# Kernel optimization log

Hardware: AMD Instinct MI355X
Metric: run time of the kernel (lower is better)

The kernel has to match this reference:

```python
import jax, jax.numpy as jnp
import numpy as np

B, C, H, W = 16, 256, 32, 32
DIM = H * W  # LayerNorm/Linear dim == h*w per the rearrange in forward


def _conv1x1(x, w, b):
    # x: [b,c,h,w], w: [out,in] (1x1 kernel squeezed), b: [out]
    return jnp.einsum('bchw,oc->bohw', x, w) + b[None, :, None, None]


def _layernorm(x, g, b, eps=1e-5):
    mu = jnp.mean(x, axis=-1, keepdims=True)
    var = jnp.var(x, axis=-1, keepdims=True)
    return (x - mu) / jnp.sqrt(var + eps) * g + b


def setup_inputs() -> dict:
    key = jax.random.key(0)
    ks = jax.random.split(key, 12)
    n = jax.random.normal
    k_cdc = (2.0 / (2 * C)) ** 0.5   # kaiming_normal fan_in = 2C
    k_v = (2.0 / C) ** 0.5           # fan_in = C
    k_lin = (2.0 / DIM) ** 0.5       # fan_in = DIM
    return {
        'x_spa': n(ks[0], (B, C, H, W), jnp.float32),
        'x_freq': n(ks[1], (B, C, H, W), jnp.float32),
        'w_cdc': n(ks[2], (C, 2 * C), jnp.float32) * k_cdc,
        'b_cdc': jnp.zeros((C,), jnp.float32),
        'w_sv': n(ks[3], (C, C), jnp.float32) * k_v,
        'b_sv': jnp.zeros((C,), jnp.float32),
        'w_fv': n(ks[4], (C, C), jnp.float32) * k_v,
        'b_fv': jnp.zeros((C,), jnp.float32),
        'ln_w': jnp.ones((DIM,), jnp.float32),
        'ln_b': jnp.zeros((DIM,), jnp.float32),
        'w_qk': n(ks[5], (2 * DIM, DIM), jnp.float32) * k_lin,  # Linear(dim, 2*dim), no bias
        'w_spa': n(ks[6], (DIM, DIM), jnp.float32) * k_lin,
        'b_spa': jnp.zeros((DIM,), jnp.float32),
        'w_frq': n(ks[7], (DIM, DIM), jnp.float32) * k_lin,
        'b_frq': jnp.zeros((DIM,), jnp.float32),
    }


def reference(x_spa, x_freq, w_cdc, b_cdc, w_sv, b_sv, w_fv, b_fv,
              ln_w, ln_b, w_qk, w_spa, b_spa, w_frq, b_frq):
    b, c, h, w = x_spa.shape
    hw = h * w
    scale = hw ** (-0.5)
    v_spa = _conv1x1(x_spa, w_sv, b_sv).reshape(b, c, hw)
    v_freq = _conv1x1(x_freq, w_fv, b_fv).reshape(b, c, hw)
    x = _conv1x1(jnp.concatenate([x_spa, x_freq], axis=1), w_cdc, b_cdc).reshape(b, c, hw)
    x = _layernorm(x, ln_w, ln_b)
    qk = x @ w_qk.T                       # [b, c, 2*hw]
    q, k = jnp.split(qk, 2, axis=-1)      # each [b, c, hw]
    att = jnp.einsum('bcn,bcm->bnm', q, k) * scale   # q^T k over channels: [b, hw, hw]
    att_spa = jax.nn.softmax(att @ w_spa.T + b_spa, axis=-1)
    att_frq = jax.nn.softmax(att @ w_frq.T + b_frq, axis=-1)
    out_spa = x_spa + jnp.einsum('bcn,bnm->bcm', v_spa, att_spa).reshape(b, c, h, w)
    out_freq = x_freq + jnp.einsum('bcn,bnm->bcm', v_freq, att_frq).reshape(b, c, h, w)
    return out_spa, out_freq
```

## Files before the change

kernel.cpp:

```cpp
#include <hip/hip_runtime.h>
#include <hip/hip_bf16.h>

typedef __hip_bfloat16 bf16;
typedef __attribute__((ext_vector_type(8))) short bf16x8v;
typedef __attribute__((ext_vector_type(4))) float f32x4v;

__device__ __forceinline__ float bfbits2f(unsigned short h) {
    union { unsigned int u; float f; } v; v.u = ((unsigned int)h) << 16; return v.f;
}
__device__ __forceinline__ unsigned short f2bfbits(float f) {
    bf16 h = __float2bfloat16(f);
    unsigned short s;
    __builtin_memcpy(&s, &h, 2);
    return s;
}
__device__ __forceinline__ float load1_any(const void* p, long idx, bool f32) {
    if (f32) return ((const float*)p)[idx];
    return bfbits2f(((const unsigned short*)p)[idx]);
}
__device__ __forceinline__ float4 loadbf4(const bf16* p) {
    ushort4 u = *reinterpret_cast<const ushort4*>(p);
    return make_float4(bfbits2f(u.x), bfbits2f(u.y), bfbits2f(u.z), bfbits2f(u.w));
}
__device__ __forceinline__ void store_bf4(bf16* p, float a, float b, float c, float d) {
    ushort4 o;
    o.x = f2bfbits(a); o.y = f2bfbits(b); o.z = f2bfbits(c); o.w = f2bfbits(d);
    *reinterpret_cast<ushort4*>(p) = o;
}
__device__ __forceinline__ void gl16(const void* g, void* l) {
    __builtin_amdgcn_global_load_lds(
        (const __attribute__((address_space(1))) unsigned int*)g,
        (__attribute__((address_space(3))) unsigned int*)l, 16, 0, 0);
}
#define CMAX_INIT 0x00800000u

__global__ __launch_bounds__(1024)
void detect_kernel(const unsigned short* __restrict__ x, int* __restrict__ flag) {
    const int tid = threadIdx.x;
    int zc = 0, hc = 0;
    const uint4* xv = (const uint4*)x;
#pragma unroll
    for (int p = 0; p < 16; ++p) {
        uint4 v = xv[p * 1024 + tid];
        unsigned s0 = v.x & 0xFFFFu, s1 = v.y & 0xFFFFu;
        unsigned s2 = v.z & 0xFFFFu, s3 = v.w & 0xFFFFu;
        zc += (int)(s0 == 0) + (int)(s1 == 0) + (int)(s2 == 0) + (int)(s3 == 0);
        hc += (int)(((s0 >> 7) & 0xFFu) >= 0x90u) + (int)(((s1 >> 7) & 0xFFu) >= 0x90u)
            + (int)(((s2 >> 7) & 0xFFu) >= 0x90u) + (int)(((s3 >> 7) & 0xFFu) >= 0x90u);
    }
#pragma unroll
    for (int off = 32; off > 0; off >>= 1) {
        zc += __shfl_down(zc, off);
        hc += __shfl_down(hc, off);
    }
    __shared__ int rz[16], rh[16];
    if ((tid & 63) == 0) { rz[tid >> 6] = zc; rh[tid >> 6] = hc; }
    __syncthreads();
    if (tid == 0) {
        int Z = 0, H = 0;
#pragma unroll
        for (int i = 0; i < 16; ++i) { Z += rz[i]; H += rh[i]; }
        flag[0] = (Z > 60000 || H > 256) ? 1 : 0;
        flag[1] = 1;
    }
}

__global__ void diag_kernel(float* __restrict__ out, float val) {
    if (threadIdx.x == 0) out[0] = val;
}

__global__ __launch_bounds__(256)
void convert6_kernel(const void* __restrict__ s0, const void* __restrict__ s1,
                     const void* __restrict__ s2, const void* __restrict__ s3,
                     const void* __restrict__ s4, const void* __restrict__ s5,
                     const void* __restrict__ b0, const void* __restrict__ b1,
                     const void* __restrict__ b2,
                     bf16* __restrict__ dst, bf16* __restrict__ wl,
                     float* __restrict__ bc, const int* __restrict__ dflag) {
    const bool f32 = (*dflag != 0);
    for (long i = (long)blockIdx.x * 256 + threadIdx.x; i < 4850432;
         i += (long)gridDim.x * 256) {
        if (i < 4456448) {
            const void* s; long o;
            if (i < 131072)       { s = s0; o = i; }
            else if (i < 196608)  { s = s1; o = i - 131072; }
            else if (i < 262144)  { s = s2; o = i - 196608; }
            else if (i < 2359296) { s = s3; o = i - 262144; }
            else if (i < 3407872) { s = s4; o = i - 2359296; }
            else                  { s = s5; o = i - 3407872; }
            dst[i] = __float2bfloat16(load1_any(s, o, f32));
        } else if (i < 4849664) {
            long j = i - 4456448;
            int r = (int)(j >> 9), c = (int)(j & 511);
            float v = 0.f;
            if (r < 256) v = load1_any(s0, r * 512 + c, f32);
            else if (r < 512) { if (c < 256) v = load1_any(s1, (r - 256) * 256 + c, f32); }
            else              { if (c >= 256) v = load1_any(s2, (r - 512) * 256 + (c - 256), f32); }
            wl[j] = __float2bfloat16(v);
        } else {
            long j = i - 4849664;
            float v = (j < 256) ? load1_any(b0, j, f32)
                    : (j < 512) ? load1_any(b1, j - 256, f32)
                                : load1_any(b2, j - 512, f32);
            bc[j] = v;
        }
    }
}

__global__ __launch_bounds__(256)
void xpose_w_kernel(const bf16* __restrict__ src, bf16* __restrict__ dst) {
    __shared__ float t[64][65];
    const int c0 = blockIdx.x * 64, r0 = blockIdx.y * 64;
    const int tid = threadIdx.x;
#pragma unroll
    for (int p = 0; p < 16; ++p) {
        int e = tid + p * 256; int r = e >> 6, c = e & 63;
        t[r][c] = __bfloat162float(src[(long)(r0 + r) * 1024 + c0 + c]);
    }
    __syncthreads();
#pragma unroll
    for (int p = 0; p < 16; ++p) {
        int e = tid + p * 256; int r = e >> 6, c = e & 63;
        dst[(long)(c0 + r) * 1024 + r0 + c] = __float2bfloat16(t[c][r]);
    }
}

__global__ __launch_bounds__(256)
void xpose_conv_kernel(const void* __restrict__ x1, const void* __restrict__ x2,
                       bf16* __restrict__ dst, unsigned* __restrict__ colmax,
                       int bofs, int zsplit, const int* __restrict__ dflag) {
    const bool f32 = (*dflag != 0);
    __shared__ float t[64][65];
    const int ch0 = blockIdx.y * 64, n0 = blockIdx.x * 64, z = blockIdx.z;
    const bool hiz = (z >= zsplit);
    const int zl = hiz ? z - zsplit : z;
    const void* x = hiz ? x2 : x1;
    const long sb = (long)(zl + bofs) * 262144, db = (long)z * 262144;
    const int tid = threadIdx.x;
    if (blockIdx.x == 0 && blockIdx.y == 0) {
        uint4* ci = (uint4*)(colmax + (long)z * 1024) + tid;
        *ci = make_uint4(CMAX_INIT, CMAX_INIT, CMAX_INIT, CMAX_INIT);
    }
    if (f32) {
        const float* xf = (const float*)x;
#pragma unroll
        for (int p = 0; p < 4; ++p) {
            int e = tid + p * 256; int sch = e >> 4, sn = (e & 15) * 4;
            float4 v = *(const float4*)(xf + sb + (long)(ch0 + sch) * 1024 + n0 + sn);
            t[sch][sn] = v.x; t[sch][sn + 1] = v.y;
            t[sch][sn + 2] = v.z; t[sch][sn + 3] = v.w;
        }
    } else {
#pragma unroll
        for (int p = 0; p < 16; ++p) {
            int e = tid + p * 256; int sch = e >> 6, sn = e & 63;
            t[sch][sn] = bfbits2f(((const unsigned short*)x)[sb + (long)(ch0 + sch) * 1024 + n0 + sn]);
        }
    }
    __syncthreads();
#pragma unroll
    for (int p = 0; p < 16; ++p) {
        int e = tid + p * 256; int dn = e >> 6, dch = e & 63;
        dst[db + (long)(n0 + dn) * 256 + ch0 + dch] = __float2bfloat16(t[dch][dn]);
    }
}

__global__ __launch_bounds__(256)
void smnorm_kernel(bf16* __restrict__ X, bf16* __restrict__ vb,
                   const unsigned* __restrict__ colmax, int gN, int gq) {
    const int tid = threadIdx.x;
    const int cg = tid & 7;
    const int js = tid >> 3;
    const int n0 = blockIdx.x * 64;
    const long zb = (long)blockIdx.y * 1048576;
    unsigned short* Xp = (unsigned short*)X + zb + n0 + cg * 8;
    const unsigned* cm = colmax + (long)blockIdx.y * 1024 + n0 + cg * 8;

    float M8[8], s8[8];
#pragma unroll
    for (int q = 0; q < 8; ++q) {
        unsigned k = cm[q];
        unsigned b = (k & 0x80000000u) ? (k & 0x7fffffffu) : ~k;
        M8[q] = __uint_as_float(b);
        s8[q] = 0.f;
    }
#pragma unroll 4
    for (int r = 0; r < 32; ++r) {
        long off = (long)(js * 32 + r) * 1024;
        bf16x8v u = *(const bf16x8v*)(Xp + off);
        bf16x8v o;
#pragma unroll
        for (int q = 0; q < 8; ++q) {
            float e = __expf(bfbits2f((unsigned short)u[q]) - M8[q]);
            s8[q] += e;
            o[q] = (short)f2bfbits(e);
        }
        *(bf16x8v*)(Xp + off) = o;
    }
    __shared__ float sh[32][8][8];
    __shared__ float Sc[64];
#pragma unroll
    for (int q = 0; q < 8; ++q) sh[js][cg][q] = s8[q];
    __syncthreads();
    if (tid < 64) {
        float ss = 0.f;
#pragma unroll 8
        for (int s = 0; s < 32; ++s) ss += sh[s][tid >> 3][tid & 7];
        Sc[tid] = 1.0f / ss;
    }
    __syncthreads();
    const int side = (blockIdx.y >= (unsigned)gq) ? 1 : 0;
    const int zl = blockIdx.y - side * gq;
    bf16* vp = vb + (long)(side * 256) * gN + (long)zl * 1024 + n0 + cg * 8;
    float is8[8];
#pragma unroll
    for (int q = 0; q < 8; ++q) is8[q] = Sc[cg * 8 + q];
#pragma unroll
    for (int rr = 0; rr < 8; ++rr) {
        long off = (long)(rr * 32 + js) * gN;
        bf16x8v u = *(bf16x8v*)(vp + off);
        bf16x8v o;
#pragma unroll
        for (int q = 0; q < 8; ++q)
            o[q] = (short)f2bfbits(bfbits2f((unsigned short)u[q]) * is8[q]);
        *(bf16x8v*)(vp + off) = o;
    }
}

template <int MI, int EPI>
__global__ __launch_bounds__(256)
void mfma_nt(const bf16* __restrict__ A1, const bf16* __restrict__ A2,
             long aB1, long aB2, int ldA1, int ldA2,
             const bf16* __restrict__ B1, const bf16* __restrict__ B2,
             long bB1, long bB2, int ldB1, int ldB2,
             int ksplit, long kOff2,
             void* __restrict__ out1, void* __restrict__ out2,
             long oB1, long oB2, int ldO1, int ldO2,
             int K, float scale,
             const void* __restrict__ bias1, const void* __restrict__ bias2,
             const void* __restrict__ res1, const void* __restrict__ res2,
             long rBatch, int bofs, int zsplit,
             const int* __restrict__ dflag) {
    constexpr int BM = MI * 32;
    __shared__ short As[3][BM * 32];
    __shared__ short Bs[3][4096];
    const int tid  = threadIdx.x;
    const int lane = tid & 63, wave = tid >> 6;
    const int quad = lane >> 4, lrow = lane & 15;
    const int wm = (wave >> 1) * (MI * 16), wn = (wave & 1) * 64;

    int bx = blockIdx.x, by = blockIdx.y, bz = blockIdx.z;
    {
        const int gx = gridDim.x, gy = gridDim.y;
        const int gxy = gx * gy;
        const int ntot = gxy * gridDim.z;
        if ((ntot & 7) == 0) {
            int flat = bx + gx * (by + gy * bz);
            int w = (flat & 7) * (ntot >> 3) + (flat >> 3);
            bz = w / gxy;
            int rem = w - bz * gxy;
            by = rem / gx;
            bx = rem - by * gx;
        }
    }
    const int z  = bz;
    const bool hiz = (z >= zsplit);
    const int zl = hiz ? z - zsplit : z;
    const int n0 = bx * 128, m0 = by * BM;
    const int ldA = hiz ? ldA2 : ldA1, ldB = hiz ? ldB2 : ldB1;
    const int ldO = hiz ? ldO2 : ldO1;
    const int srow = tid >> 2, sseg = tid & 3;
    const int sl = sseg ^ ((srow >> 1) & 3);
    const int xq = quad ^ ((lrow >> 1) & 3);

    const bf16* Ab = (hiz ? A2 : A1) + (long)zl * (hiz ? aB2 : aB1);
    const bf16* Bb = (hiz ? B2 : B1) + (long)zl * (hiz ? bB2 : bB1);

    auto stage = [&](int buf, int k0) {
        const bf16* asrc = Ab + (long)k0;
        const bf16* bsrc = Bb + ((k0 < ksplit) ? (long)k0 : (long)(k0 - ksplit) + kOff2);
#pragma unroll
        for (int p = 0; p < MI / 2; ++p)
            gl16(asrc + (long)(m0 + p * 64 + srow) * ldA + sl * 8,
                 &As[buf][p * 2048 + wave * 512]);
        gl16(bsrc + (long)(n0 + srow) * ldB + sl * 8, &Bs[buf][wave * 512]);
        gl16(bsrc + (long)(n0 + 64 + srow) * ldB + sl * 8, &Bs[buf][2048 + wave * 512]);
    };

    f32x4v acc[MI][4] = {};
    const int nt = K >> 5;
    stage(0, 0);
    if (nt > 1) stage(1, 32);

    int cur = 0;
    for (int t = 0; t < nt; ++t) {
        if (t + 1 < nt) {
            if constexpr (MI == 4) asm volatile("s_waitcnt vmcnt(4)" ::: "memory");
            else                   asm volatile("s_waitcnt vmcnt(3)" ::: "memory");
        } else {
            asm volatile("s_waitcnt vmcnt(0)" ::: "memory");
        }
        __builtin_amdgcn_s_barrier();
        __builtin_amdgcn_sched_barrier(0);
        if (t + 2 < nt) {
            int nb = cur + 2; if (nb >= 3) nb -= 3;
            stage(nb, (t + 2) << 5);
        }
        bf16x8v bfr[4], afr[MI];
#pragma unroll
        for (int j = 0; j < 4; ++j)
            bfr[j] = *(const bf16x8v*)&Bs[cur][(wn + j * 16 + lrow) * 32 + xq * 8];
#pragma unroll
        for (int i = 0; i < MI; ++i)
            afr[i] = *(const bf16x8v*)&As[cur][(wm + i * 16 + lrow) * 32 + xq * 8];
        __builtin_amdgcn_s_setprio(1);
#pragma unroll
        for (int i = 0; i < MI; ++i)
#pragma unroll
            for (int j = 0; j < 4; ++j)
                acc[i][j] = __builtin_amdgcn_mfma_f32_16x16x32_bf16(afr[i], bfr[j], acc[i][j], 0, 0, 0);
        __builtin_amdgcn_s_setprio(0);
        cur = (cur == 2) ? 0 : cur + 1;
    }

    const bool f32 = (*dflag != 0);
    const void* bias = hiz ? bias2 : bias1;
    if (EPI != 3) {
        bf16* O = (bf16*)(hiz ? out2 : out1) + (long)zl * (hiz ? oB2 : oB1);
        float colm[4] = {-3.4e38f, -3.4e38f, -3.4e38f, -3.4e38f};
#pragma unroll
        for (int i = 0; i < MI; ++i) {
            int row0 = m0 + wm + i * 16 + quad * 4;
            float rb[4] = {0.f, 0.f, 0.f, 0.f};
            if (EPI == 1 || EPI == 2) {
#pragma unroll
                for (int r = 0; r < 4; ++r) rb[r] = load1_any(bias, row0 + r, f32);
            }
#pragma unroll
            for (int j = 0; j < 4; ++j) {
                int col = n0 + wn + j * 16 + lrow;
#pragma unroll
                for (int r = 0; r < 4; ++r) {
                    float vv = acc[i][j][r];
                    if (EPI == 1) vv += rb[r];
                    if (EPI == 2) { vv = vv * scale + rb[r]; colm[j] = fmaxf(colm[j], vv); }
                    O[(long)(row0 + r) * ldO + col] = __float2bfloat16(vv);
                }
            }
        }
        if constexpr (EPI == 2) {
            __shared__ float smx[2][128];
#pragma unroll
            for (int off = 16; off < 64; off <<= 1)
#pragma unroll
                for (int j = 0; j < 4; ++j)
                    colm[j] = fmaxf(colm[j], __shfl_xor(colm[j], off));
            if (quad == 0) {
#pragma unroll
                for (int j = 0; j < 4; ++j)
                    smx[wave >> 1][wn + j * 16 + lrow] = colm[j];
            }
            __syncthreads();
            if (tid < 128) {
                float M = fmaxf(smx[0][tid], smx[1][tid]);
                unsigned b = __float_as_uint(M);
                unsigned key = (b & 0x80000000u) ? ~b : (b | 0x80000000u);
                unsigned* cmp = (unsigned*)(hiz ? res2 : res1) + (long)zl * rBatch + n0 + tid;
                atomicMax(cmp, key);
            }
        }
    } else {
        float* O = (float*)(hiz ? out2 : out1);
        const void* res = hiz ? res2 : res1;
        const long ob  = (long)(zl + bofs) * (hiz ? oB2 : oB1);
        const long rbb = (long)(zl + bofs) * rBatch;
#pragma unroll
        for (int i = 0; i < MI; ++i) {
            int row0 = m0 + wm + i * 16 + quad * 4;
#pragma unroll
            for (int j = 0; j < 4; ++j) {
                int col = n0 + wn + j * 16 + lrow;
#pragma unroll
                for (int r = 0; r < 4; ++r) {
                    float rv = load1_any(res, rbb + (long)(row0 + r) * ldO + col, f32);
                    O[ob + (long)(row0 + r) * ldO + col] = acc[i][j][r] + rv;
                }
            }
        }
    }
}

__global__ __launch_bounds__(256)
void layernorm_kernel(const bf16* __restrict__ src, bf16* __restrict__ dst,
                      const void* __restrict__ g, const void* __restrict__ beta,
                      int gN, const int* __restrict__ dflag) {
    const bool f32 = (*dflag != 0);
    const int zc = blockIdx.x;
    const int zz = zc >> 8, c = zc & 255;
    const bf16* p = src + (long)c * gN + (long)zz * 1024;
    bf16* q = dst + (long)zc * 1024;
    const int tid = threadIdx.x;
    float4 v = loadbf4(p + tid * 4);
    float s  = v.x + v.y + v.z + v.w;
    float ss = v.x * v.x + v.y * v.y + v.z * v.z + v.w * v.w;
#pragma unroll
    for (int off = 32; off > 0; off >>= 1) {
        s  += __shfl_down(s, off);
        ss += __shfl_down(ss, off);
    }
    __shared__ float sh[8];
    __shared__ float sh_mu, sh_rs;
    if ((tid & 63) == 0) { sh[tid >> 6] = s; sh[4 + (tid >> 6)] = ss; }
    __syncthreads();
    if (tid == 0) {
        float S  = sh[0] + sh[1] + sh[2] + sh[3];
        float SS = sh[4] + sh[5] + sh[6] + sh[7];
        float mu = S * (1.0f / 1024.0f);
        float var = SS * (1.0f / 1024.0f) - mu * mu;
        sh_mu = mu;
        sh_rs = rsqrtf(fmaxf(var, 0.0f) + 1e-5f);
    }
    __syncthreads();
    float mu = sh_mu, rs = sh_rs;
    float gx = load1_any(g, tid * 4 + 0, f32), gy = load1_any(g, tid * 4 + 1, f32);
    float gz = load1_any(g, tid * 4 + 2, f32), gw = load1_any(g, tid * 4 + 3, f32);
    float bx = load1_any(beta, tid * 4 + 0, f32), by = load1_any(beta, tid * 4 + 1, f32);
    float bz = load1_any(beta, tid * 4 + 2, f32), bw = load1_any(beta, tid * 4 + 3, f32);
    store_bf4(q + tid * 4,
              (v.x - mu) * rs * gx + bx, (v.y - mu) * rs * gy + by,
              (v.z - mu) * rs * gz + bz, (v.w - mu) * rs * gw + bw);
}

extern "C" void kernel_launch(void* const* d_in, const int* in_sizes, int n_in,
                              void* d_out, int out_size, void* d_ws, size_t ws_size,
                              hipStream_t stream) {
    const void* x_spa  = d_in[0];
    const void* x_freq = d_in[1];
    const void* w_cdc  = d_in[2];
    const void* b_cdc  = d_in[3];
    const void* w_sv   = d_in[4];
    const void* b_sv   = d_in[5];
    const void* w_fv   = d_in[6];
    const void* b_fv   = d_in[7];
    const void* ln_w   = d_in[8];
    const void* ln_b   = d_in[9];
    const void* w_qk   = d_in[10];
    const void* w_spa  = d_in[11];
    const void* b_spa  = d_in[12];
    const void* w_frq  = d_in[13];
    const void* b_frq  = d_in[14];
    float* out = (float*)d_out;

    const int B = 16, C = 256;
    const long XB = 262144;
    const long PB = 1048576;

    int*   dflag = (int*)d_ws;
    float* bcat  = (float*)((char*)d_ws + 1024);
    bf16*  wb    = (bf16*)((char*)d_ws + 4096);
    bf16* w_cdc_b = wb;
    bf16* w_sv_b  = w_cdc_b + 131072;
    bf16* w_fv_b  = w_sv_b  + 65536;
    bf16* w_qk_b  = w_fv_b  + 65536;
    bf16* w_spa_b = w_qk_b  + 2097152;
    bf16* w_frq_b = w_spa_b + 1048576;
    bf16* w_qk_hiT= w_frq_b + 1048576;
    bf16* W1f     = w_qk_hiT + 1048576;
    bf16* Wleft   = W1f + 1048576;
    bf16* pb      = Wleft + 393216;

    const size_t fixedB = 4096 + 6946816ull * 2;
    const size_t perB   = 8921088ull;
    size_t avail = (ws_size > fixedB) ? (ws_size - fixedB) : 0;
    long gmax = (long)(avail / perB);
    const bool wsOK = (gmax >= 1);
    int G = wsOK ? (int)(gmax > 16 ? 16 : gmax) : 1;

    bf16* xT    = pb;
    bf16* XV    = xT  + 2L * G * XB;
    bf16* xln2  = XV  + 3L * G * XB;
    bf16* qTT   = xln2 + (long)G * XB;
    bf16* attpT = qTT + 3L * G * XB;
    unsigned* colmax = (unsigned*)(attpT + 2L * G * PB);

    dim3 blk(256);
    detect_kernel<<<dim3(1), dim3(1024), 0, stream>>>((const unsigned short*)x_spa, dflag);

    if (!wsOK) {
        float mb = (float)(ws_size >> 20);
        diag_kernel<<<dim3(1), dim3(64), 0, stream>>>(out, 1000.0f * (mb + 1.0f));
        return;
    }

    convert6_kernel<<<dim3(4352), blk, 0, stream>>>(
        w_cdc, w_sv, w_fv, w_qk, w_spa, w_frq, b_cdc, b_sv, b_fv,
        wb, Wleft, bcat, dflag);
    xpose_w_kernel<<<dim3(16, 16), blk, 0, stream>>>(w_qk_b + 1048576, w_qk_hiT);
    mfma_nt<4, 0><<<dim3(8, 8, 2), blk, 0, stream>>>(
        w_spa_b, w_frq_b, 0, 0, 1024, 1024,
        w_qk_hiT, w_qk_hiT, 0, 0, 1024, 1024, 1024, 0,
        w_qk_b + 1048576, W1f, 0, 0, 1024, 1024,
        1024, 1.0f, nullptr, nullptr, nullptr, nullptr, 0, 0, 1, dflag);

    for (int b0 = 0; b0 < B; b0 += G) {
        int g = (B - b0 < G) ? (B - b0) : G;
        const int gN = g * 1024;
        bf16* vb = XV + 256L * gN;

        xpose_conv_kernel<<<dim3(16, 4, 2 * g), blk, 0, stream>>>(
            x_spa, x_freq, xT, colmax, b0, g, dflag);

        mfma_nt<4, 1><<<dim3(8 * g, 6, 1), blk, 0, stream>>>(
            Wleft, Wleft, 0, 0, 512, 512,
            xT, xT, 0, 0, 256, 256, 256, (long)g * XB,
            XV, XV, 0, 0, gN, gN,
            512, 1.0f, bcat, bcat, nullptr, nullptr, 0, 0, 1, dflag + 1);

        layernorm_kernel<<<dim3(g * C), blk, 0, stream>>>(XV, xln2, ln_w, ln_b, gN, dflag);

        mfma_nt<4, 0><<<dim3(2 * g, 8, 3), blk, 0, stream>>>(
            w_qk_b, W1f, 1048576, 0, 1024, 1024,
            xln2, xln2, 0, 0, 1024, 1024, 1024, 0,
            qTT, qTT + 2L * g * XB, (long)g * XB, 0, g * 256, g * 256,
            1024, 1.0f, nullptr, nullptr, nullptr, nullptr, 0, 0, 2, dflag);

        mfma_nt<4, 2><<<dim3(8, 8, 2 * g), blk, 0, stream>>>(
            qTT + (long)g * XB, qTT + 2L * g * XB, 256, 256, g * 256, g * 256,
            qTT, qTT, 256, 256, g * 256, g * 256, 256, 0,
            attpT, attpT + (long)g * PB, PB, PB, 1024, 1024,
            256, 0.03125f, b_spa, b_frq, colmax, colmax + (long)g * 1024,
            1024, 0, g, dflag);

        smnorm_kernel<<<dim3(16, 2 * g), blk, 0, stream>>>(attpT, vb, colmax, gN, g);

        mfma_nt<4, 3><<<dim3(8, 2, 2 * g), blk, 0, stream>>>(
            vb, vb + 256L * gN, 1024, 1024, gN, gN,
            attpT, attpT + (long)g * PB, PB, PB, 1024, 1024, 1024, 0,
            out, out + 4194304, XB, XB, 1024, 1024,
            1024, 1.0f, nullptr, nullptr, x_spa, x_freq, XB, b0, g, dflag);
    }
}
```

Baseline: 336.9 us.

## Add two-tile-per-barrier double-buffered K loop variant for selected GEMMs

Adds a template flag that switches the MFMA GEMM main loop from a 3-stage ring with one barrier per 32-wide K tile to a 4-buffer scheme. That scheme loads two K tiles at once and computes two tiles per barrier. It is enabled for the weight-fold GEMM, the attention-score GEMM and the final V·attention GEMM. The goal is to halve barrier and waitcnt overhead per K step. The cost is more LDS (4 buffers instead of 3), which may reduce occupancy. It also waits for all outstanding loads (vmcnt(0)) each iteration, which could weaken load/compute overlap.

```diff
diff --git a/kernel.cpp b/kernel.cpp
--- a/kernel.cpp
+++ b/kernel.cpp
@@ -227,11 +227,11 @@
     }
 }
 
-template <int MI, int EPI>
+template <int MI, int EPI, bool B2>
 __global__ __launch_bounds__(256)
 void mfma_nt(const bf16* __restrict__ A1, const bf16* __restrict__ A2,
              long aB1, long aB2, int ldA1, int ldA2,
-             const bf16* __restrict__ B1, const bf16* __restrict__ B2,
+             const bf16* __restrict__ B1, const bf16* __restrict__ B2p,
              long bB1, long bB2, int ldB1, int ldB2,
              int ksplit, long kOff2,
              void* __restrict__ out1, void* __restrict__ out2,
@@ -242,8 +242,9 @@
              long rBatch, int bofs, int zsplit,
              const int* __restrict__ dflag) {
     constexpr int BM = MI * 32;
-    __shared__ short As[3][BM * 32];
-    __shared__ short Bs[3][4096];
+    constexpr int NBUF = B2 ? 4 : 3;
+    __shared__ short As[NBUF][BM * 32];
+    __shared__ short Bs[NBUF][4096];
     const int tid  = threadIdx.x;
     const int lane = tid & 63, wave = tid >> 6;
     const int quad = lane >> 4, lrow = lane & 15;
@@ -274,7 +275,7 @@
     const int xq = quad ^ ((lrow >> 1) & 3);
 
     const bf16* Ab = (hiz ? A2 : A1) + (long)zl * (hiz ? aB2 : aB1);
-    const bf16* Bb = (hiz ? B2 : B1) + (long)zl * (hiz ? bB2 : bB1);
+    const bf16* Bb = (hiz ? B2p : B1) + (long)zl * (hiz ? bB2 : bB1);
 
     auto stage = [&](int buf, int k0) {
         const bf16* asrc = Ab + (long)k0;
@@ -286,26 +287,7 @@
         gl16(bsrc + (long)(n0 + srow) * ldB + sl * 8, &Bs[buf][wave * 512]);
         gl16(bsrc + (long)(n0 + 64 + srow) * ldB + sl * 8, &Bs[buf][2048 + wave * 512]);
     };
-
-    f32x4v acc[MI][4] = {};
-    const int nt = K >> 5;
-    stage(0, 0);
-    if (nt > 1) stage(1, 32);
-
-    int cur = 0;
-    for (int t = 0; t < nt; ++t) {
-        if (t + 1 < nt) {
-            if constexpr (MI == 4) asm volatile("s_waitcnt vmcnt(4)" ::: "memory");
-            else                   asm volatile("s_waitcnt vmcnt(3)" ::: "memory");
-        } else {
-            asm volatile("s_waitcnt vmcnt(0)" ::: "memory");
-        }
-        __builtin_amdgcn_s_barrier();
-        __builtin_amdgcn_sched_barrier(0);
-        if (t + 2 < nt) {
-            int nb = cur + 2; if (nb >= 3) nb -= 3;
-            stage(nb, (t + 2) << 5);
-        }
+    auto compute = [&](int cur, f32x4v (&acc)[MI][4]) {
         bf16x8v bfr[4], afr[MI];
 #pragma unroll
         for (int j = 0; j < 4; ++j)
@@ -320,7 +302,48 @@
             for (int j = 0; j < 4; ++j)
                 acc[i][j] = __builtin_amdgcn_mfma_f32_16x16x32_bf16(afr[i], bfr[j], acc[i][j], 0, 0, 0);
         __builtin_amdgcn_s_setprio(0);
-        cur = (cur == 2) ? 0 : cur + 1;
+    };
+
+    f32x4v acc[MI][4] = {};
+    const int nt = K >> 5;
+
+    if constexpr (B2) {
+        stage(0, 0);
+        stage(1, 32);
+        const int nw = nt >> 1;
+        for (int w = 0; w < nw; ++w) {
+            asm volatile("s_waitcnt vmcnt(0)" ::: "memory");
+            __builtin_amdgcn_s_barrier();
+            __builtin_amdgcn_sched_barrier(0);
+            const int cb = (w & 1) ? 2 : 0;
+            const int sb = (w & 1) ? 0 : 2;
+            if (w + 1 < nw) {
+                stage(sb, (2 * w + 2) << 5);
+                stage(sb + 1, (2 * w + 3) << 5);
+            }
+            compute(cb, acc);
+            compute(cb + 1, acc);
+        }
+    } else {
+        stage(0, 0);
+        if (nt > 1) stage(1, 32);
+        int cur = 0;
+        for (int t = 0; t < nt; ++t) {
+            if (t + 1 < nt) {
+                if constexpr (MI == 4) asm volatile("s_waitcnt vmcnt(4)" ::: "memory");
+                else                   asm volatile("s_waitcnt vmcnt(3)" ::: "memory");
+            } else {
+                asm volatile("s_waitcnt vmcnt(0)" ::: "memory");
+            }
+            __builtin_amdgcn_s_barrier();
+            __builtin_amdgcn_sched_barrier(0);
+            if (t + 2 < nt) {
+                int nb = cur + 2; if (nb >= 3) nb -= 3;
+                stage(nb, (t + 2) << 5);
+            }
+            compute(cur, acc);
+            cur = (cur == 2) ? 0 : cur + 1;
+        }
     }
 
     const bool f32 = (*dflag != 0);
@@ -496,7 +519,7 @@
         w_cdc, w_sv, w_fv, w_qk, w_spa, w_frq, b_cdc, b_sv, b_fv,
         wb, Wleft, bcat, dflag);
     xpose_w_kernel<<<dim3(16, 16), blk, 0, stream>>>(w_qk_b + 1048576, w_qk_hiT);
-    mfma_nt<4, 0><<<dim3(8, 8, 2), blk, 0, stream>>>(
+    mfma_nt<4, 0, true><<<dim3(8, 8, 2), blk, 0, stream>>>(
         w_spa_b, w_frq_b, 0, 0, 1024, 1024,
         w_qk_hiT, w_qk_hiT, 0, 0, 1024, 1024, 1024, 0,
         w_qk_b + 1048576, W1f, 0, 0, 1024, 1024,
@@ -510,7 +533,7 @@
         xpose_conv_kernel<<<dim3(16, 4, 2 * g), blk, 0, stream>>>(
             x_spa, x_freq, xT, colmax, b0, g, dflag);
 
-        mfma_nt<4, 1><<<dim3(8 * g, 6, 1), blk, 0, stream>>>(
+        mfma_nt<4, 1, false><<<dim3(8 * g, 6, 1), blk, 0, stream>>>(
             Wleft, Wleft, 0, 0, 512, 512,
             xT, xT, 0, 0, 256, 256, 256, (long)g * XB,
             XV, XV, 0, 0, gN, gN,
@@ -518,13 +541,13 @@
 
         layernorm_kernel<<<dim3(g * C), blk, 0, stream>>>(XV, xln2, ln_w, ln_b, gN, dflag);
 
-        mfma_nt<4, 0><<<dim3(2 * g, 8, 3), blk, 0, stream>>>(
+        mfma_nt<4, 0, false><<<dim3(2 * g, 8, 3), blk, 0, stream>>>(
             w_qk_b, W1f, 1048576, 0, 1024, 1024,
             xln2, xln2, 0, 0, 1024, 1024, 1024, 0,
             qTT, qTT + 2L * g * XB, (long)g * XB, 0, g * 256, g * 256,
             1024, 1.0f, nullptr, nullptr, nullptr, nullptr, 0, 0, 2, dflag);
 
-        mfma_nt<4, 2><<<dim3(8, 8, 2 * g), blk, 0, stream>>>(
+        mfma_nt<4, 2, true><<<dim3(8, 8, 2 * g), blk, 0, stream>>>(
             qTT + (long)g * XB, qTT + 2L * g * XB, 256, 256, g * 256, g * 256,
             qTT, qTT, 256, 256, g * 256, g * 256, 256, 0,
             attpT, attpT + (long)g * PB, PB, PB, 1024, 1024,
@@ -533,7 +556,7 @@
 
         smnorm_kernel<<<dim3(16, 2 * g), blk, 0, stream>>>(attpT, vb, colmax, gN, g);
 
-        mfma_nt<4, 3><<<dim3(8, 2, 2 * g), blk, 0, stream>>>(
+        mfma_nt<4, 3, true><<<dim3(8, 2, 2 * g), blk, 0, stream>>>(
             vb, vb + 256L * gN, 1024, 1024, gN, gN,
             attpT, attpT + (long)g * PB, PB, PB, 1024, 1024, 1024, 0,
             out, out + 4194304, XB, XB, 1024, 1024,
```

Measured after the change: 334.1 us. No clear change (-0.8%).
